# Performance work log

Measured on AMD Instinct MI355X. Metric: run time of the kernel, lower is better.

Reference implementation:

```python
import jax, jax.numpy as jnp
import numpy as np

B, C, H, W = 8, 1152, 32, 32
N = H * W


def _skew(t):
    # t: (B,3) -> (B,3,3) skew-symmetric
    z = jnp.zeros_like(t[:, 0])
    return jnp.stack([
        jnp.stack([z, -t[:, 2], t[:, 1]], axis=-1),
        jnp.stack([t[:, 2], z, -t[:, 0]], axis=-1),
        jnp.stack([-t[:, 1], t[:, 0], z], axis=-1),
    ], axis=1)


def _fundamental(K1, K2, R, t):
    E = _skew(t) @ R
    U, S, Vt = jnp.linalg.svd(E)
    S = S.at[:, 2].set(0.0)  # enforce rank-2 essential matrix
    E = U @ (S[:, :, None] * Vt)
    return jnp.linalg.inv(jnp.swapaxes(K2, 1, 2)) @ E @ jnp.linalg.inv(K1)


def setup_inputs() -> dict:
    key = jax.random.key(0)
    k1, k2, k3, k4, k5 = jax.random.split(key, 5)
    f_tar = jax.random.normal(k1, (B, C, H, W), dtype=jnp.float32)
    f_src = jax.random.normal(k2, (B, C, H, W), dtype=jnp.float32)
    # realistic invertible intrinsics: [[fx,0,cx],[0,fy,cy],[0,0,1]]
    def intrinsics(k):
        f = 30.0 + 2.0 * jax.random.uniform(k, (B, 2))
        Kt = jnp.zeros((B, 3, 3))
        Kt = Kt.at[:, 0, 0].set(f[:, 0]).at[:, 1, 1].set(f[:, 1])
        Kt = Kt.at[:, 0, 2].set(W / 2.0).at[:, 1, 2].set(H / 2.0).at[:, 2, 2].set(1.0)
        return Kt.astype(jnp.float32)
    K1 = intrinsics(k3)
    K2 = intrinsics(k4)
    # proper rotation via QR of a random matrix
    ka, kb = jax.random.split(k5)
    Q, Rm = jnp.linalg.qr(jax.random.normal(ka, (B, 3, 3)))
    Q = Q * jnp.sign(jnp.diagonal(Rm, axis1=1, axis2=2))[:, None, :]
    Q = Q * jnp.linalg.det(Q)[:, None, None]  # det = +1
    t = jax.random.normal(kb, (B, 3), dtype=jnp.float32)
    return {"f_tar": f_tar, "f_src": f_src, "K1": K1, "K2": K2,
            "R": Q.astype(jnp.float32), "t": t}


def reference(f_tar, f_src, K1, K2, R, t):
    f_src_flat = f_src.reshape(B, C, N)  # (B,C,N)
    # NOTE: torch code computes A = f_src^T @ f_tar but never uses it (dead code); omitted.

    # homogeneous pixel coords, indexing='ij': x=row index, y=col index
    ix, iy = jnp.meshgrid(jnp.arange(H, dtype=jnp.float32),
                          jnp.arange(W, dtype=jnp.float32), indexing='ij')
    combined = jnp.stack([ix.ravel(), iy.ravel(), jnp.ones(N, jnp.float32)], axis=0)  # (3,N)
    combined = jnp.broadcast_to(combined, (B, 3, N))

    F_mat = _fundamental(K1, K2, R, t)                       # (B,3,3)
    lines = F_mat @ combined                                 # (B,3,N)
    lines = lines / lines[:, 2:3, :]

    ones = jnp.ones((B, 1, N), jnp.float32)
    x0 = jnp.zeros((B, 1, N), jnp.float32)
    y0 = -lines[:, 2:3, :] / lines[:, 1:2, :]
    point_0 = jnp.concatenate([x0, y0, ones], axis=1)        # (B,3,N)
    x1 = jnp.full((B, 1, N), float(W), jnp.float32)
    y1 = -(lines[:, 2:3, :] + lines[:, 0:1, :] * W) / lines[:, 1:2, :]
    point_1 = jnp.concatenate([x1, y1, ones], axis=1)        # (B,3,N)

    # point-to-line distance for every (pixel i, line j) pair -> (B,N,N)
    diff = point_0 - point_1                                 # (B,3,N)
    p = combined[:, :, :, None] - point_0[:, :, None, :]     # (B,3,N,N) via broadcast
    d = diff[:, :, None, :]                                  # (B,3,1,N)
    cross = jnp.stack([
        p[:, 1] * d[:, 2] - p[:, 2] * d[:, 1],
        p[:, 2] * d[:, 0] - p[:, 0] * d[:, 2],
        p[:, 0] * d[:, 1] - p[:, 1] * d[:, 0],
    ], axis=1)                                               # (B,3,N,N)
    cross_norm = jnp.sqrt(jnp.sum(cross * cross, axis=1))    # (B,N,N)
    diff_norm = jnp.linalg.norm(diff, axis=1, keepdims=True) # (B,1,N)
    d_epi = cross_norm / diff_norm                           # (B,N,N)

    thre = 0.1
    weight_map = 1.0 - jax.nn.softmax(5.0 * (d_epi - thre), axis=-1)
    attention_map = jax.nn.softmax(weight_map, axis=1)       # softmax over dim=1, per torch code

    out = jnp.einsum('bij,bjc->bic', attention_map, jnp.swapaxes(f_src_flat, 1, 2))  # (B,N,C)
    return out.reshape(B, C, H, W)
```

## Files before the change

### kernel.cpp

```cpp
#include <hip/hip_runtime.h>
#include <hip/hip_bf16.h>
#include <math.h>

#define Bn 8
#define Cn 1152
#define Hn 32
#define Wn 32
#define Nn 1024

typedef short short8 __attribute__((ext_vector_type(8)));
typedef float f32x4 __attribute__((ext_vector_type(4)));

__device__ float g_dy[Bn * Nn];
__device__ float g_y0[Bn * Nn];
__device__ float g_invn[Bn * Nn];
__device__ float g_rmax[Bn * Nn];
__device__ float g_rsuminv[Bn * Nn];
__device__ float g_csum[Bn * Nn];
__device__ unsigned short g_A[(size_t)Bn * Nn * Nn];
__device__ unsigned short g_fb[(size_t)Bn * Cn * Nn];

__device__ inline unsigned short f2bf(float x) {
    __hip_bfloat16 h = __float2bfloat16(x);
    unsigned short u;
    __builtin_memcpy(&u, &h, 2);
    return u;
}

__device__ inline void inv3(const float* M, float* o) {
    float a = M[0], b = M[1], c = M[2];
    float d = M[3], e = M[4], f = M[5];
    float g = M[6], h = M[7], i = M[8];
    float A0 = (e * i - f * h);
    float A1 = -(d * i - f * g);
    float A2 = (d * h - e * g);
    float det = a * A0 + b * A1 + c * A2;
    float inv = 1.0f / det;
    o[0] = A0 * inv;
    o[1] = -(b * i - c * h) * inv;
    o[2] = (b * f - c * e) * inv;
    o[3] = A1 * inv;
    o[4] = (a * i - c * g) * inv;
    o[5] = -(a * f - c * d) * inv;
    o[6] = A2 * inv;
    o[7] = -(a * h - b * g) * inv;
    o[8] = (a * e - b * d) * inv;
}

__device__ inline void mm3(const float* X, const float* Y, float* Z) {
    for (int r = 0; r < 3; r++)
        for (int c = 0; c < 3; c++)
            Z[r * 3 + c] = X[r * 3 + 0] * Y[0 * 3 + c] + X[r * 3 + 1] * Y[1 * 3 + c] +
                           X[r * 3 + 2] * Y[2 * 3 + c];
}

__global__ void setup_kernel(const float* __restrict__ K1, const float* __restrict__ K2,
                             const float* __restrict__ R, const float* __restrict__ t) {
    __shared__ float Fs[9];
    int b = blockIdx.x;
    for (int j = threadIdx.x; j < Nn; j += blockDim.x) g_csum[b * Nn + j] = 0.0f;
    if (threadIdx.x == 0) {
        float t0 = t[b * 3 + 0], t1 = t[b * 3 + 1], t2 = t[b * 3 + 2];
        float S[9] = {0.0f, -t2, t1, t2, 0.0f, -t0, -t1, t0, 0.0f};
        float E[9];
        mm3(S, &R[b * 9], E);
        float iK1[9], iK2[9];
        inv3(&K1[b * 9], iK1);
        inv3(&K2[b * 9], iK2);
        float iK2T[9] = {iK2[0], iK2[3], iK2[6], iK2[1], iK2[4], iK2[7], iK2[2], iK2[5], iK2[8]};
        float T[9], F[9];
        mm3(iK2T, E, T);
        mm3(T, iK1, F);
        for (int k = 0; k < 9; k++) Fs[k] = F[k];
    }
    __syncthreads();
    for (int j = threadIdx.x; j < Nn; j += blockDim.x) {
        float ix = (float)(j >> 5);
        float iy = (float)(j & 31);
        float l0 = Fs[0] * ix + Fs[1] * iy + Fs[2];
        float l1 = Fs[3] * ix + Fs[4] * iy + Fs[5];
        float l2 = Fs[6] * ix + Fs[7] * iy + Fs[8];
        l0 = l0 / l2;
        l1 = l1 / l2;
        float y0 = -1.0f / l1;
        float y1 = -(1.0f + l0 * 32.0f) / l1;
        float dy = y0 - y1;
        float dn = sqrtf(1024.0f + dy * dy);
        g_dy[b * Nn + j] = dy;
        g_y0[b * Nn + j] = y0;
        g_invn[b * Nn + j] = 1.0f / dn;
    }
}

__device__ inline float zval(float ix, float iy, float dy, float y0, float invn) {
    float d = fabsf(ix * dy + 32.0f * (iy - y0)) * invn;
    return 5.0f * (d - 0.1f);
}

__global__ void rowstats_kernel() {
    int lin = blockIdx.x;
    int b = lin & 7;
    int seg = lin >> 3;
    int wv = threadIdx.x >> 6;
    int lane = threadIdx.x & 63;
    int i = seg * 4 + wv;
    float ix = (float)(i >> 5), iy = (float)(i & 31);
    int base = b * Nn;
    float z[16];
    float m = -INFINITY;
#pragma unroll
    for (int k = 0; k < 16; k++) {
        int j = lane + k * 64;
        z[k] = zval(ix, iy, g_dy[base + j], g_y0[base + j], g_invn[base + j]);
        m = fmaxf(m, z[k]);
    }
#pragma unroll
    for (int o = 32; o > 0; o >>= 1) m = fmaxf(m, __shfl_xor(m, o, 64));
    float s = 0.0f;
#pragma unroll
    for (int k = 0; k < 16; k++) s += __expf(z[k] - m);
#pragma unroll
    for (int o = 32; o > 0; o >>= 1) s += __shfl_xor(s, o, 64);
    if (lane == 0) {
        g_rmax[base + i] = m;
        g_rsuminv[base + i] = 1.0f / s;
    }
}

__global__ void colE_kernel() {
    int lin = blockIdx.x;
    int b = lin & 7;
    int r = lin >> 3;
    int jc = r & 3;
    int iseg = r >> 2;
    int t = threadIdx.x;
    int j = jc * 256 + t;
    int base = b * Nn;
    float dy = g_dy[base + j], y0 = g_y0[base + j], invn = g_invn[base + j];
    float csum = 0.0f;
    for (int k = 0; k < 128; k++) {
        int i = iseg * 128 + k;
        float rmax = g_rmax[base + i];
        float rsuminv = g_rsuminv[base + i];
        float ix = (float)(i >> 5), iy = (float)(i & 31);
        float z = zval(ix, iy, dy, y0, invn);
        float s1 = __expf(z - rmax) * rsuminv;
        float E = __expf(1.0f - s1);
        csum += E;
        g_A[((size_t)base + i) * Nn + j] = f2bf(E);
    }
    atomicAdd(&g_csum[base + j], csum);
}

__global__ void convert_fsrc_kernel(const float* __restrict__ f) {
    int lin = blockIdx.x;
    int b = lin & 7;
    int rrow = lin >> 3;
    int local = rrow * 1024 + threadIdx.x * 4;
    int j = threadIdx.x * 4;
    size_t off = (size_t)b * Cn * Nn + local;
    float4 v = *(const float4*)(f + off);
    float4 cs = *(const float4*)&g_csum[b * Nn + j];
    ushort4 u;
    u.x = f2bf(v.x / cs.x);
    u.y = f2bf(v.y / cs.y);
    u.z = f2bf(v.z / cs.z);
    u.w = f2bf(v.w / cs.w);
    *(ushort4*)&g_fb[off] = u;
}

#define BM 128
#define BNc 128
#define BK 32

__launch_bounds__(256) __global__ void gemm_kernel(float* __restrict__ out) {
    __shared__ unsigned short As[BM * BK];
    __shared__ unsigned short Bs[BNc * BK];
    int lin = blockIdx.x;
    int b = lin & 7;
    int s = lin >> 3;
    int it = s / 9;
    int ct = s - it * 9;
    int i0 = it * BM;
    int c0 = ct * BNc;
    int t = threadIdx.x;
    int w = t >> 6, L = t & 63;
    int wm = w >> 1, wn = w & 1;
    const unsigned short* Ab = g_A + (size_t)b * Nn * Nn + (size_t)i0 * Nn;
    const unsigned short* Fb = g_fb + (size_t)b * Cn * Nn + (size_t)c0 * Nn;
    f32x4 acc[4][4] = {};
    for (int kt = 0; kt < Nn; kt += BK) {
        __syncthreads();
#pragma unroll
        for (int h = 0; h < 2; h++) {
            int chunk = (h * 4 + w) * 64 + L;
            int r = chunk >> 2;
            int gq = (chunk & 3) ^ ((r >> 1) & 3);
            const unsigned short* ga = Ab + (size_t)r * Nn + kt + gq * 8;
            const unsigned short* gb = Fb + (size_t)r * Nn + kt + gq * 8;
            __builtin_amdgcn_global_load_lds(
                (const __attribute__((address_space(1))) unsigned int*)ga,
                (__attribute__((address_space(3))) unsigned int*)(As + chunk * 8), 16, 0, 0);
            __builtin_amdgcn_global_load_lds(
                (const __attribute__((address_space(1))) unsigned int*)gb,
                (__attribute__((address_space(3))) unsigned int*)(Bs + chunk * 8), 16, 0, 0);
        }
        __syncthreads();
        short8 af[4], bf[4];
        int lrow = L & 15, quad = L >> 4;
#pragma unroll
        for (int mt = 0; mt < 4; mt++) {
            int r = wm * 64 + mt * 16 + lrow;
            int q = quad ^ ((r >> 1) & 3);
            af[mt] = *(const short8*)(As + r * BK + q * 8);
        }
#pragma unroll
        for (int nt = 0; nt < 4; nt++) {
            int r = wn * 64 + nt * 16 + lrow;
            int q = quad ^ ((r >> 1) & 3);
            bf[nt] = *(const short8*)(Bs + r * BK + q * 8);
        }
#pragma unroll
        for (int mt = 0; mt < 4; mt++)
#pragma unroll
            for (int nt = 0; nt < 4; nt++)
                acc[mt][nt] =
                    __builtin_amdgcn_mfma_f32_16x16x32_bf16(af[mt], bf[nt], acc[mt][nt], 0, 0, 0);
    }
    int col = L & 15, quad = L >> 4;
#pragma unroll
    for (int mt = 0; mt < 4; mt++)
#pragma unroll
        for (int rg = 0; rg < 4; rg++) {
            int i = i0 + wm * 64 + mt * 16 + quad * 4 + rg;
            float* orow = out + ((size_t)b * Nn + i) * Cn + c0 + wn * 64;
#pragma unroll
            for (int nt = 0; nt < 4; nt++) orow[nt * 16 + col] = acc[mt][nt][rg];
        }
}

extern "C" void kernel_launch(void* const* d_in, const int* in_sizes, int n_in,
                              void* d_out, int out_size, void* d_ws, size_t ws_size,
                              hipStream_t stream) {
    (void)in_sizes; (void)n_in; (void)d_ws; (void)ws_size; (void)out_size;
    const float* f_src = (const float*)d_in[1];
    const float* K1 = (const float*)d_in[2];
    const float* K2 = (const float*)d_in[3];
    const float* R = (const float*)d_in[4];
    const float* t = (const float*)d_in[5];
    float* out = (float*)d_out;

    setup_kernel<<<dim3(Bn), dim3(256), 0, stream>>>(K1, K2, R, t);
    rowstats_kernel<<<dim3(2048), dim3(256), 0, stream>>>();
    colE_kernel<<<dim3(256), dim3(256), 0, stream>>>();
    convert_fsrc_kernel<<<dim3(Bn * Cn), dim3(256), 0, stream>>>(f_src);
    gemm_kernel<<<dim3(Bn * (Nn / BM) * (Cn / BNc)), dim3(256), 0, stream>>>(out);
}
```

Measured before the change: 190.5 us.

## Drop setup kernel, recompute line params inline, double-buffer GEMM LDS, partial column sums

Removes the setup kernel by recomputing the fundamental matrix and per-pixel line parameters inside rowstats and colE, which saves a launch and the global round trips for the line parameters. colE gets a finer 1024-block grid, and its atomic column sums become per-tile partial sums reduced in shared memory, then summed in the conversion kernel. The GEMM double-buffers its LDS tiles so the next k-tile's loads are issued before the current tile's MFMAs. The cost is redundant arithmetic per thread and twice the LDS for the GEMM.

```diff
diff --git a/kernel.cpp b/kernel.cpp
--- a/kernel.cpp
+++ b/kernel.cpp
@@ -11,12 +11,9 @@
 typedef short short8 __attribute__((ext_vector_type(8)));
 typedef float f32x4 __attribute__((ext_vector_type(4)));
 
-__device__ float g_dy[Bn * Nn];
-__device__ float g_y0[Bn * Nn];
-__device__ float g_invn[Bn * Nn];
 __device__ float g_rmax[Bn * Nn];
 __device__ float g_rsuminv[Bn * Nn];
-__device__ float g_csum[Bn * Nn];
+__device__ float g_csum_part[Bn * 8 * Nn];
 __device__ unsigned short g_A[(size_t)Bn * Nn * Nn];
 __device__ unsigned short g_fb[(size_t)Bn * Cn * Nn];
 
@@ -54,42 +51,33 @@
                            X[r * 3 + 2] * Y[2 * 3 + c];
 }
 
-__global__ void setup_kernel(const float* __restrict__ K1, const float* __restrict__ K2,
-                             const float* __restrict__ R, const float* __restrict__ t) {
-    __shared__ float Fs[9];
-    int b = blockIdx.x;
-    for (int j = threadIdx.x; j < Nn; j += blockDim.x) g_csum[b * Nn + j] = 0.0f;
-    if (threadIdx.x == 0) {
-        float t0 = t[b * 3 + 0], t1 = t[b * 3 + 1], t2 = t[b * 3 + 2];
-        float S[9] = {0.0f, -t2, t1, t2, 0.0f, -t0, -t1, t0, 0.0f};
-        float E[9];
-        mm3(S, &R[b * 9], E);
-        float iK1[9], iK2[9];
-        inv3(&K1[b * 9], iK1);
-        inv3(&K2[b * 9], iK2);
-        float iK2T[9] = {iK2[0], iK2[3], iK2[6], iK2[1], iK2[4], iK2[7], iK2[2], iK2[5], iK2[8]};
-        float T[9], F[9];
-        mm3(iK2T, E, T);
-        mm3(T, iK1, F);
-        for (int k = 0; k < 9; k++) Fs[k] = F[k];
-    }
-    __syncthreads();
-    for (int j = threadIdx.x; j < Nn; j += blockDim.x) {
-        float ix = (float)(j >> 5);
-        float iy = (float)(j & 31);
-        float l0 = Fs[0] * ix + Fs[1] * iy + Fs[2];
-        float l1 = Fs[3] * ix + Fs[4] * iy + Fs[5];
-        float l2 = Fs[6] * ix + Fs[7] * iy + Fs[8];
-        l0 = l0 / l2;
-        l1 = l1 / l2;
-        float y0 = -1.0f / l1;
-        float y1 = -(1.0f + l0 * 32.0f) / l1;
-        float dy = y0 - y1;
-        float dn = sqrtf(1024.0f + dy * dy);
-        g_dy[b * Nn + j] = dy;
-        g_y0[b * Nn + j] = y0;
-        g_invn[b * Nn + j] = 1.0f / dn;
-    }
+__device__ inline void computeF(const float* K1, const float* K2, const float* R,
+                                const float* t, int b, float* F) {
+    float t0 = t[b * 3 + 0], t1 = t[b * 3 + 1], t2 = t[b * 3 + 2];
+    float S[9] = {0.0f, -t2, t1, t2, 0.0f, -t0, -t1, t0, 0.0f};
+    float E[9];
+    mm3(S, &R[b * 9], E);
+    float iK1[9], iK2[9];
+    inv3(&K1[b * 9], iK1);
+    inv3(&K2[b * 9], iK2);
+    float iK2T[9] = {iK2[0], iK2[3], iK2[6], iK2[1], iK2[4], iK2[7], iK2[2], iK2[5], iK2[8]};
+    float T[9];
+    mm3(iK2T, E, T);
+    mm3(T, iK1, F);
+}
+
+__device__ inline void lineparams(const float* F, int j, float& dy, float& y0, float& invn) {
+    float ix = (float)(j >> 5);
+    float iy = (float)(j & 31);
+    float l0 = F[0] * ix + F[1] * iy + F[2];
+    float l1 = F[3] * ix + F[4] * iy + F[5];
+    float l2 = F[6] * ix + F[7] * iy + F[8];
+    l0 = l0 / l2;
+    l1 = l1 / l2;
+    y0 = -1.0f / l1;
+    float y1 = -(1.0f + l0 * 32.0f) / l1;
+    dy = y0 - y1;
+    invn = 1.0f / sqrtf(1024.0f + dy * dy);
 }
 
 __device__ inline float zval(float ix, float iy, float dy, float y0, float invn) {
@@ -97,21 +85,25 @@
     return 5.0f * (d - 0.1f);
 }
 
-__global__ void rowstats_kernel() {
+__global__ void rowstats_kernel(const float* __restrict__ K1, const float* __restrict__ K2,
+                                const float* __restrict__ R, const float* __restrict__ t) {
     int lin = blockIdx.x;
     int b = lin & 7;
     int seg = lin >> 3;
+    float F[9];
+    computeF(K1, K2, R, t, b, F);
     int wv = threadIdx.x >> 6;
     int lane = threadIdx.x & 63;
     int i = seg * 4 + wv;
     float ix = (float)(i >> 5), iy = (float)(i & 31);
-    int base = b * Nn;
     float z[16];
     float m = -INFINITY;
 #pragma unroll
     for (int k = 0; k < 16; k++) {
         int j = lane + k * 64;
-        z[k] = zval(ix, iy, g_dy[base + j], g_y0[base + j], g_invn[base + j]);
+        float dy, y0, invn;
+        lineparams(F, j, dy, y0, invn);
+        z[k] = zval(ix, iy, dy, y0, invn);
         m = fmaxf(m, z[k]);
     }
 #pragma unroll
@@ -122,45 +114,62 @@
 #pragma unroll
     for (int o = 32; o > 0; o >>= 1) s += __shfl_xor(s, o, 64);
     if (lane == 0) {
-        g_rmax[base + i] = m;
-        g_rsuminv[base + i] = 1.0f / s;
-    }
-}
-
-__global__ void colE_kernel() {
+        g_rmax[b * Nn + i] = m;
+        g_rsuminv[b * Nn + i] = 1.0f / s;
+    }
+}
+
+__global__ void colE_kernel(const float* __restrict__ K1, const float* __restrict__ K2,
+                            const float* __restrict__ R, const float* __restrict__ t) {
     int lin = blockIdx.x;
     int b = lin & 7;
     int r = lin >> 3;
-    int jc = r & 3;
-    int iseg = r >> 2;
-    int t = threadIdx.x;
-    int j = jc * 256 + t;
+    int jt = r & 15;
+    int it = r >> 4;
+    float F[9];
+    computeF(K1, K2, R, t, b, F);
+    int tt = threadIdx.x;
+    int jloc = tt & 63;
+    int ig = tt >> 6;
+    int j = jt * 64 + jloc;
     int base = b * Nn;
-    float dy = g_dy[base + j], y0 = g_y0[base + j], invn = g_invn[base + j];
-    float csum = 0.0f;
-    for (int k = 0; k < 128; k++) {
-        int i = iseg * 128 + k;
+    float dy, y0, invn;
+    lineparams(F, j, dy, y0, invn);
+    float csump = 0.0f;
+#pragma unroll 4
+    for (int k = 0; k < 32; k++) {
+        int i = it * 128 + ig * 32 + k;
         float rmax = g_rmax[base + i];
-        float rsuminv = g_rsuminv[base + i];
+        float rsi = g_rsuminv[base + i];
         float ix = (float)(i >> 5), iy = (float)(i & 31);
         float z = zval(ix, iy, dy, y0, invn);
-        float s1 = __expf(z - rmax) * rsuminv;
+        float s1 = __expf(z - rmax) * rsi;
         float E = __expf(1.0f - s1);
-        csum += E;
+        csump += E;
         g_A[((size_t)base + i) * Nn + j] = f2bf(E);
     }
-    atomicAdd(&g_csum[base + j], csum);
+    __shared__ float red[4][64];
+    red[ig][jloc] = csump;
+    __syncthreads();
+    if (ig == 0) {
+        float s = red[0][jloc] + red[1][jloc] + red[2][jloc] + red[3][jloc];
+        g_csum_part[(b * 8 + it) * Nn + j] = s;
+    }
 }
 
 __global__ void convert_fsrc_kernel(const float* __restrict__ f) {
     int lin = blockIdx.x;
     int b = lin & 7;
-    int rrow = lin >> 3;
-    int local = rrow * 1024 + threadIdx.x * 4;
+    int c = lin >> 3;
     int j = threadIdx.x * 4;
-    size_t off = (size_t)b * Cn * Nn + local;
+    float4 cs = *(const float4*)&g_csum_part[(b * 8 + 0) * Nn + j];
+#pragma unroll
+    for (int it = 1; it < 8; it++) {
+        float4 p = *(const float4*)&g_csum_part[(b * 8 + it) * Nn + j];
+        cs.x += p.x; cs.y += p.y; cs.z += p.z; cs.w += p.w;
+    }
+    size_t off = ((size_t)b * Cn + c) * Nn + j;
     float4 v = *(const float4*)(f + off);
-    float4 cs = *(const float4*)&g_csum[b * Nn + j];
     ushort4 u;
     u.x = f2bf(v.x / cs.x);
     u.y = f2bf(v.y / cs.y);
@@ -174,8 +183,8 @@
 #define BK 32
 
 __launch_bounds__(256) __global__ void gemm_kernel(float* __restrict__ out) {
-    __shared__ unsigned short As[BM * BK];
-    __shared__ unsigned short Bs[BNc * BK];
+    __shared__ unsigned short As[2][BM * BK];
+    __shared__ unsigned short Bs[2][BNc * BK];
     int lin = blockIdx.x;
     int b = lin & 7;
     int s = lin >> 3;
@@ -188,37 +197,43 @@
     int wm = w >> 1, wn = w & 1;
     const unsigned short* Ab = g_A + (size_t)b * Nn * Nn + (size_t)i0 * Nn;
     const unsigned short* Fb = g_fb + (size_t)b * Cn * Nn + (size_t)c0 * Nn;
-    f32x4 acc[4][4] = {};
-    for (int kt = 0; kt < Nn; kt += BK) {
-        __syncthreads();
+
+    auto stage = [&](int p, int kt) {
 #pragma unroll
         for (int h = 0; h < 2; h++) {
             int chunk = (h * 4 + w) * 64 + L;
-            int r = chunk >> 2;
-            int gq = (chunk & 3) ^ ((r >> 1) & 3);
-            const unsigned short* ga = Ab + (size_t)r * Nn + kt + gq * 8;
-            const unsigned short* gb = Fb + (size_t)r * Nn + kt + gq * 8;
+            int rr = chunk >> 2;
+            int gq = (chunk & 3) ^ ((rr >> 1) & 3);
+            const unsigned short* ga = Ab + (size_t)rr * Nn + kt + gq * 8;
+            const unsigned short* gb = Fb + (size_t)rr * Nn + kt + gq * 8;
             __builtin_amdgcn_global_load_lds(
                 (const __attribute__((address_space(1))) unsigned int*)ga,
-                (__attribute__((address_space(3))) unsigned int*)(As + chunk * 8), 16, 0, 0);
+                (__attribute__((address_space(3))) unsigned int*)(As[p] + chunk * 8), 16, 0, 0);
             __builtin_amdgcn_global_load_lds(
                 (const __attribute__((address_space(1))) unsigned int*)gb,
-                (__attribute__((address_space(3))) unsigned int*)(Bs + chunk * 8), 16, 0, 0);
-        }
+                (__attribute__((address_space(3))) unsigned int*)(Bs[p] + chunk * 8), 16, 0, 0);
+        }
+    };
+
+    f32x4 acc[4][4] = {};
+    int lrow = L & 15, quad = L >> 4;
+    stage(0, 0);
+    for (int kt = 0; kt < Nn; kt += BK) {
+        int p = (kt >> 5) & 1;
         __syncthreads();
+        if (kt + BK < Nn) stage(1 - p, kt + BK);
         short8 af[4], bf[4];
-        int lrow = L & 15, quad = L >> 4;
 #pragma unroll
         for (int mt = 0; mt < 4; mt++) {
-            int r = wm * 64 + mt * 16 + lrow;
-            int q = quad ^ ((r >> 1) & 3);
-            af[mt] = *(const short8*)(As + r * BK + q * 8);
+            int rr = wm * 64 + mt * 16 + lrow;
+            int q = quad ^ ((rr >> 1) & 3);
+            af[mt] = *(const short8*)(As[p] + rr * BK + q * 8);
         }
 #pragma unroll
         for (int nt = 0; nt < 4; nt++) {
-            int r = wn * 64 + nt * 16 + lrow;
-            int q = quad ^ ((r >> 1) & 3);
-            bf[nt] = *(const short8*)(Bs + r * BK + q * 8);
+            int rr = wn * 64 + nt * 16 + lrow;
+            int q = quad ^ ((rr >> 1) & 3);
+            bf[nt] = *(const short8*)(Bs[p] + rr * BK + q * 8);
         }
 #pragma unroll
         for (int mt = 0; mt < 4; mt++)
@@ -227,7 +242,6 @@
                 acc[mt][nt] =
                     __builtin_amdgcn_mfma_f32_16x16x32_bf16(af[mt], bf[nt], acc[mt][nt], 0, 0, 0);
     }
-    int col = L & 15, quad = L >> 4;
 #pragma unroll
     for (int mt = 0; mt < 4; mt++)
 #pragma unroll
@@ -235,7 +249,7 @@
             int i = i0 + wm * 64 + mt * 16 + quad * 4 + rg;
             float* orow = out + ((size_t)b * Nn + i) * Cn + c0 + wn * 64;
 #pragma unroll
-            for (int nt = 0; nt < 4; nt++) orow[nt * 16 + col] = acc[mt][nt][rg];
+            for (int nt = 0; nt < 4; nt++) orow[nt * 16 + quad * 0 + (L & 15)] = acc[mt][nt][rg];
         }
 }
 
@@ -250,9 +264,8 @@
     const float* t = (const float*)d_in[5];
     float* out = (float*)d_out;
 
-    setup_kernel<<<dim3(Bn), dim3(256), 0, stream>>>(K1, K2, R, t);
-    rowstats_kernel<<<dim3(2048), dim3(256), 0, stream>>>();
-    colE_kernel<<<dim3(256), dim3(256), 0, stream>>>();
+    rowstats_kernel<<<dim3(2048), dim3(256), 0, stream>>>(K1, K2, R, t);
+    colE_kernel<<<dim3(1024), dim3(256), 0, stream>>>(K1, K2, R, t);
     convert_fsrc_kernel<<<dim3(Bn * Cn), dim3(256), 0, stream>>>(f_src);
     gemm_kernel<<<dim3(Bn * (Nn / BM) * (Cn / BNc)), dim3(256), 0, stream>>>(out);
 }
```

After: 198.8 us. +4.4%, slower.
